# Optimization experiments

Hardware: AMD Instinct MI355X
Metric: run time of the kernel (lower is better)

## Reference

```python
import jax, jax.numpy as jnp
import numpy as np

H = 16
D_MODEL = 1024
D_K = D_MODEL // H
B, S = 2, 2048


def setup_inputs() -> dict:
    key = jax.random.key(0)
    ks = jax.random.split(key, 11)
    scale = 1.0 / np.sqrt(D_MODEL)
    inp = {
        "query": jax.random.normal(ks[0], (B, S, D_MODEL), jnp.float32),
        "key": jax.random.normal(ks[1], (B, S, D_MODEL), jnp.float32),
        "value": jax.random.normal(ks[2], (B, S, D_MODEL), jnp.float32),
        # four nn.Linear(d_model, d_model): Wq, Wk, Wv, Wo (torch convention: y = x @ W.T + b)
        "Wq": jax.random.uniform(ks[3], (D_MODEL, D_MODEL), jnp.float32, -scale, scale),
        "bq": jax.random.uniform(ks[4], (D_MODEL,), jnp.float32, -scale, scale),
        "Wk": jax.random.uniform(ks[5], (D_MODEL, D_MODEL), jnp.float32, -scale, scale),
        "bk": jax.random.uniform(ks[6], (D_MODEL,), jnp.float32, -scale, scale),
        "Wv": jax.random.uniform(ks[7], (D_MODEL, D_MODEL), jnp.float32, -scale, scale),
        "bv": jax.random.uniform(ks[8], (D_MODEL,), jnp.float32, -scale, scale),
        "Wo": jax.random.uniform(ks[9], (D_MODEL, D_MODEL), jnp.float32, -scale, scale),
        "bo": jax.random.uniform(ks[10], (D_MODEL,), jnp.float32, -scale, scale),
    }
    return inp


def _split_heads(x):
    # [B, S, D] -> [B, H, S, d_k]
    b, s, _ = x.shape
    return x.reshape(b, s, H, D_K).transpose(0, 2, 1, 3)


def reference(query, key, value, Wq, bq, Wk, bk, Wv, bv, Wo, bo):
    q = _split_heads(query @ Wq.T + bq)
    k = _split_heads(key @ Wk.T + bk)
    v = _split_heads(value @ Wv.T + bv)
    # scaled dot-product attention (dropout omitted: reference is eval-mode)
    scores = jnp.einsum("bhqd,bhkd->bhqk", q, k) / np.sqrt(D_K).astype(np.float32)
    p = jax.nn.softmax(scores, axis=-1)
    x = jnp.einsum("bhqk,bhkd->bhqd", p, v)
    x = x.transpose(0, 2, 1, 3).reshape(query.shape[0], -1, H * D_K)
    return x @ Wo.T + bo
```

## Files before the change

kernel.cpp:

```cpp
#include <hip/hip_runtime.h>

typedef unsigned short u16;
typedef unsigned int u32;
typedef __attribute__((ext_vector_type(8))) short short8;
typedef __attribute__((ext_vector_type(8))) _Float16 half8;
typedef __attribute__((ext_vector_type(4))) float floatx4;
typedef __attribute__((ext_vector_type(4))) unsigned short ushortx4;
typedef __attribute__((ext_vector_type(4))) unsigned int uint4v;

#define DEV static __device__ __forceinline__

DEV float bf2f(u16 u) { union { unsigned u; float f; } v; v.u = ((unsigned)u) << 16; return v.f; }
DEV u16 f2bf(float f) {
  union { float f; unsigned u; } v; v.f = f;
  return (u16)((v.u + 0x7FFFu + ((v.u >> 16) & 1u)) >> 16);
}
DEV u16 f2h(float f) { return __builtin_bit_cast(u16, (_Float16)f); }
DEV u32 pkh(float a, float b) {
  return __builtin_bit_cast(u32, __builtin_amdgcn_cvt_pkrtz(a, b));
}
DEV float fexp2(float x) { return __builtin_amdgcn_exp2f(x); }

#define GLDS(g, l) __builtin_amdgcn_global_load_lds( \
    (const __attribute__((address_space(1))) void*)(g), \
    (__attribute__((address_space(3))) void*)(l), 16, 0, 0)

struct CvtArg {
  const float* src[11];
  u16* dst[11];
  int cum[12];
};

__global__ void convert(CvtArg a) {
  const long base = ((long)blockIdx.x * 256 + threadIdx.x) * 4;
  if (base >= a.cum[11]) return;
  int s = 0;
  while (s < 10 && base >= a.cum[s + 1]) ++s;
  const long off = base - a.cum[s];
  const float* sp = a.src[s] + off;
  ushortx4 u;
#pragma unroll
  for (int r = 0; r < 4; ++r) u[r] = f2bf(sp[r]);
  *(ushortx4*)(a.dst[s] + off) = u;
}

struct GemmArg {
  const u16* x;
  const u16* w;
  const u16* bias;
  u16* dst;
  int mode;
};

__global__ __launch_bounds__(256, 2) void gemm_nt(GemmArg g0, GemmArg g1, GemmArg g2) {
  GemmArg g = (blockIdx.z == 0) ? g0 : ((blockIdx.z == 1) ? g1 : g2);
  __shared__ u16 As[2][128 * 32];
  __shared__ u16 Bs[2][128 * 32];
  const int tid = threadIdx.x, w = tid >> 6, l = tid & 63;
  const int l15 = l & 15, quad = l >> 4;
  const int bm = blockIdx.x, bn = blockIdx.y;
  const int wm = w >> 1, wn = w & 1;

  floatx4 acc[4][4];
#pragma unroll
  for (int i = 0; i < 4; ++i)
#pragma unroll
    for (int j = 0; j < 4; ++j) acc[i][j] = (floatx4){0.f, 0.f, 0.f, 0.f};

  const u16* xb = g.x + (long)(bm * 128 + w * 16 + (l >> 2)) * 1024 + (l & 3) * 8;
  const u16* wb = g.w + (long)(bn * 128 + w * 16 + (l >> 2)) * 1024 + (l & 3) * 8;
  const int sbo = (w * 16) * 32;

  for (int kt = 0; kt < 16; ++kt) {
    const int k0 = kt * 64;
    __syncthreads();
#pragma unroll
    for (int kc = 0; kc < 2; ++kc) {
#pragma unroll
      for (int p = 0; p < 2; ++p) {
        GLDS(xb + (long)p * 64 * 1024 + k0 + kc * 32, &As[kc][sbo + p * 64 * 32]);
        GLDS(wb + (long)p * 64 * 1024 + k0 + kc * 32, &Bs[kc][sbo + p * 64 * 32]);
      }
    }
    __syncthreads();
#pragma unroll
    for (int kc = 0; kc < 2; ++kc) {
      short8 af[4], bfr[4];
#pragma unroll
      for (int mi = 0; mi < 4; ++mi)
        af[mi] = *(const short8*)&As[kc][(wm * 64 + mi * 16 + l15) * 32 + quad * 8];
#pragma unroll
      for (int ni = 0; ni < 4; ++ni)
        bfr[ni] = *(const short8*)&Bs[kc][(wn * 64 + ni * 16 + l15) * 32 + quad * 8];
#pragma unroll
      for (int mi = 0; mi < 4; ++mi)
#pragma unroll
        for (int ni = 0; ni < 4; ++ni)
          acc[mi][ni] = __builtin_amdgcn_mfma_f32_16x16x32_bf16(af[mi], bfr[ni], acc[mi][ni], 0, 0, 0);
    }
  }

  float bv[4];
#pragma unroll
  for (int ni = 0; ni < 4; ++ni) bv[ni] = bf2f(g.bias[bn * 128 + wn * 64 + ni * 16 + l15]);

#pragma unroll
  for (int mi = 0; mi < 4; ++mi) {
    const int mbase = bm * 128 + wm * 64 + mi * 16 + quad * 4;
#pragma unroll
    for (int ni = 0; ni < 4; ++ni) {
      const int n = bn * 128 + wn * 64 + ni * 16 + l15;
      if (g.mode == 2) {
        const int b = mbase >> 11, s = mbase & 2047;
        const int h = n >> 6, d = n & 63;
        ushortx4 u;
#pragma unroll
        for (int r = 0; r < 4; ++r) u[r] = f2h(acc[mi][ni][r] + bv[ni]);
        *(ushortx4*)&g.dst[((long)(b * 16 + h) * 64 + d) * 2048 + s] = u;
      } else {
        const float sc = (g.mode == 0) ? 0.18033688011f : 1.0f;
        const int h = n >> 6, d = n & 63;
#pragma unroll
        for (int r = 0; r < 4; ++r) {
          const int m = mbase + r, b = m >> 11, s = m & 2047;
          g.dst[((long)(b * 16 + h) * 2048 + s) * 64 + d] = f2bf((acc[mi][ni][r] + bv[ni]) * sc);
        }
      }
    }
  }
}

__global__ __launch_bounds__(256, 2) void gemm_o(const u16* __restrict__ x,
                                                 const u16* __restrict__ wo,
                                                 const u16* __restrict__ bias,
                                                 float* __restrict__ dst) {
  const int bid = blockIdx.x;
  const int gidx = (bid & 7) * 64 + (bid >> 3);
  const int bm = gidx & 63;
  const int bn = gidx >> 6;

  __shared__ u16 As[2][64 * 32];
  __shared__ u16 Bs[2][128 * 32];
  const int tid = threadIdx.x, w = tid >> 6, l = tid & 63;
  const int l15 = l & 15, quad = l >> 4;
  const int wm = w >> 1, wn = w & 1;

  floatx4 acc[2][4];
#pragma unroll
  for (int i = 0; i < 2; ++i)
#pragma unroll
    for (int j = 0; j < 4; ++j) acc[i][j] = (floatx4){0.f, 0.f, 0.f, 0.f};

  const u16* xb = x + (long)(bm * 64 + w * 16 + (l >> 2)) * 1024 + (l & 3) * 8;
  const u16* wb = wo + (long)(bn * 128 + w * 16 + (l >> 2)) * 1024 + (l & 3) * 8;
  const int sbo = (w * 16) * 32;

  for (int kt = 0; kt < 16; ++kt) {
    const int k0 = kt * 64;
    __syncthreads();
#pragma unroll
    for (int kc = 0; kc < 2; ++kc) {
      GLDS(xb + k0 + kc * 32, &As[kc][sbo]);
#pragma unroll
      for (int p = 0; p < 2; ++p)
        GLDS(wb + (long)p * 64 * 1024 + k0 + kc * 32, &Bs[kc][sbo + p * 64 * 32]);
    }
    __syncthreads();
#pragma unroll
    for (int kc = 0; kc < 2; ++kc) {
      short8 af[2], bfr[4];
#pragma unroll
      for (int mi = 0; mi < 2; ++mi)
        af[mi] = *(const short8*)&As[kc][(wm * 32 + mi * 16 + l15) * 32 + quad * 8];
#pragma unroll
      for (int ni = 0; ni < 4; ++ni)
        bfr[ni] = *(const short8*)&Bs[kc][(wn * 64 + ni * 16 + l15) * 32 + quad * 8];
#pragma unroll
      for (int mi = 0; mi < 2; ++mi)
#pragma unroll
        for (int ni = 0; ni < 4; ++ni)
          acc[mi][ni] = __builtin_amdgcn_mfma_f32_16x16x32_bf16(af[mi], bfr[ni], acc[mi][ni], 0, 0, 0);
    }
  }

  float bv[4];
#pragma unroll
  for (int ni = 0; ni < 4; ++ni) bv[ni] = bf2f(bias[bn * 128 + wn * 64 + ni * 16 + l15]);

#pragma unroll
  for (int mi = 0; mi < 2; ++mi) {
    const int mbase = bm * 64 + wm * 32 + mi * 16 + quad * 4;
#pragma unroll
    for (int ni = 0; ni < 4; ++ni) {
      const int n = bn * 128 + wn * 64 + ni * 16 + l15;
#pragma unroll
      for (int r = 0; r < 4; ++r)
        dst[(long)(mbase + r) * 1024 + n] = acc[mi][ni][r] + bv[ni];
    }
  }
}

__global__ __launch_bounds__(256, 2) void attn_flash(const u16* __restrict__ Q,
                                                     const u16* __restrict__ K,
                                                     const u16* __restrict__ V,
                                                     u16* __restrict__ X) {
  __shared__ u16 KVs[4][64 * 72];
  const int tid = threadIdx.x, w = tid >> 6, l = tid & 63;
  const int l15 = l & 15, quad = l >> 4;
  const int qh = w >> 1, kh = w & 1;

  const int bid = blockIdx.x;
  const int xcd = bid & 7, idx = bid >> 3;
  const int qx = idx & 15, bh = xcd + 8 * (idx >> 4);
  const int q0 = qx * 128;

  const u16* qp = Q + (long)bh * 2048 * 64;
  const u16* kp = K + (long)bh * 2048 * 64;
  const u16* vp = V + (long)bh * 2048 * 64;

  const int r0 = tid >> 3, c0 = tid & 7, r1 = 32 + (tid >> 3);

  short8 skA0, svA0, skA1, svA1, skB0, svB0, skB1, svB1;

#define ISSUE_LOADS_A(kv0) \
    skA0 = *(const short8*)(kp + (long)((kv0) + r0) * 64 + c0 * 8); \
    svA0 = *(const short8*)(vp + (long)r0 * 2048 + (kv0) + c0 * 8); \
    skA1 = *(const short8*)(kp + (long)((kv0) + r1) * 64 + c0 * 8); \
    svA1 = *(const short8*)(vp + (long)r1 * 2048 + (kv0) + c0 * 8);

#define ISSUE_LOADS_B(kv0) \
    skB0 = *(const short8*)(kp + (long)((kv0) + r0) * 64 + c0 * 8); \
    svB0 = *(const short8*)(vp + (long)r0 * 2048 + (kv0) + c0 * 8); \
    skB1 = *(const short8*)(kp + (long)((kv0) + r1) * 64 + c0 * 8); \
    svB1 = *(const short8*)(vp + (long)r1 * 2048 + (kv0) + c0 * 8);

#define STORE_TILE_A(pb_) \
    *(short8*)&KVs[pb_][r0 * 72 + c0 * 8] = skA0; \
    *(short8*)&KVs[2 + (pb_)][r0 * 72 + c0 * 8] = svA0; \
    *(short8*)&KVs[pb_][r1 * 72 + c0 * 8] = skA1; \
    *(short8*)&KVs[2 + (pb_)][r1 * 72 + c0 * 8] = svA1;

#define STORE_TILE_B(pb_) \
    *(short8*)&KVs[pb_][r0 * 72 + c0 * 8] = skB0; \
    *(short8*)&KVs[2 + (pb_)][r0 * 72 + c0 * 8] = svB0; \
    *(short8*)&KVs[pb_][r1 * 72 + c0 * 8] = skB1; \
    *(short8*)&KVs[2 + (pb_)][r1 * 72 + c0 * 8] = svB1;

  short8 qf[4][2];
#pragma unroll
  for (int nq = 0; nq < 4; ++nq)
#pragma unroll
    for (int kc = 0; kc < 2; ++kc)
      qf[nq][kc] = *(const short8*)(qp + (long)(q0 + qh * 64 + nq * 16 + l15) * 64 + kc * 32 + quad * 8);

  floatx4 o[4][4];
#pragma unroll
  for (int nq = 0; nq < 4; ++nq)
#pragma unroll
    for (int nd = 0; nd < 4; ++nd) o[nq][nd] = (floatx4){0.f, 0.f, 0.f, 0.f};
  float den[4] = {0.f, 0.f, 0.f, 0.f};

  const bool p1 = (l & 32) != 0;
  const bool p3 = (l & 16) != 0;
  const bool p2 = p1 ^ p3;

#define BFLY(pbv, m00, m01, m10, m11) { \
    u32 A0 = p1 ? (m10) : (m00), A1 = p1 ? (m11) : (m01); \
    u32 s0_ = p1 ? (m00) : (m10), s1_ = p1 ? (m01) : (m11); \
    u32 B0 = (u32)__shfl_xor((int)s0_, 32), B1 = (u32)__shfl_xor((int)s1_, 32); \
    u32 t0 = p2 ? A0 : B0, t1 = p2 ? A1 : B1; \
    u32 u0 = (u32)__shfl_xor((int)t0, 16), u1 = (u32)__shfl_xor((int)t1, 16); \
    u32 w0 = p2 ? B0 : A0, w1 = p2 ? B1 : A1; \
    pbv[0] = p3 ? u0 : w0; pbv[1] = p3 ? u1 : w1; \
    pbv[2] = p3 ? w0 : u0; pbv[3] = p3 ? w1 : u1; \
  }

#define ATTN_ITER(t, p, IS, ST) { \
    if ((t) < 30) { IS(((t) + 2) * 64) } \
    if ((t) < 31) { ST((p) ^ 1) } \
    const int kr0 = kh * 32 + l15, kr1 = kh * 32 + 16 + l15; \
    short8 ak00 = *(const short8*)&KVs[p][kr0 * 72 + quad * 8]; \
    short8 ak01 = *(const short8*)&KVs[p][kr0 * 72 + 32 + quad * 8]; \
    short8 ak10 = *(const short8*)&KVs[p][kr1 * 72 + quad * 8]; \
    short8 ak11 = *(const short8*)&KVs[p][kr1 * 72 + 32 + quad * 8]; \
    half8 vf0 = *(const half8*)&KVs[2 + (p)][(0 * 16 + l15) * 72 + kh * 32 + quad * 8]; \
    half8 vf1 = *(const half8*)&KVs[2 + (p)][(1 * 16 + l15) * 72 + kh * 32 + quad * 8]; \
    half8 vf2 = *(const half8*)&KVs[2 + (p)][(2 * 16 + l15) * 72 + kh * 32 + quad * 8]; \
    half8 vf3 = *(const half8*)&KVs[2 + (p)][(3 * 16 + l15) * 72 + kh * 32 + quad * 8]; \
    u32 pk[4][2][2]; \
    _Pragma("unroll") \
    for (int nq = 0; nq < 4; ++nq) { \
      floatx4 st0 = (floatx4){0.f, 0.f, 0.f, 0.f}, st1 = (floatx4){0.f, 0.f, 0.f, 0.f}; \
      st0 = __builtin_amdgcn_mfma_f32_16x16x32_bf16(ak00, qf[nq][0], st0, 0, 0, 0); \
      st0 = __builtin_amdgcn_mfma_f32_16x16x32_bf16(ak01, qf[nq][1], st0, 0, 0, 0); \
      st1 = __builtin_amdgcn_mfma_f32_16x16x32_bf16(ak10, qf[nq][0], st1, 0, 0, 0); \
      st1 = __builtin_amdgcn_mfma_f32_16x16x32_bf16(ak11, qf[nq][1], st1, 0, 0, 0); \
      float e0 = fexp2(st0[0]), e1 = fexp2(st0[1]), e2 = fexp2(st0[2]), e3 = fexp2(st0[3]); \
      den[nq] += (e0 + e1) + (e2 + e3); \
      pk[nq][0][0] = pkh(e0, e1); pk[nq][0][1] = pkh(e2, e3); \
      e0 = fexp2(st1[0]); e1 = fexp2(st1[1]); e2 = fexp2(st1[2]); e3 = fexp2(st1[3]); \
      den[nq] += (e0 + e1) + (e2 + e3); \
      pk[nq][1][0] = pkh(e0, e1); pk[nq][1][1] = pkh(e2, e3); \
    } \
    _Pragma("unroll") \
    for (int nq = 0; nq < 4; ++nq) { \
      uint4v pb; \
      BFLY(pb, pk[nq][0][0], pk[nq][0][1], pk[nq][1][0], pk[nq][1][1]) \
      half8 pbs = __builtin_bit_cast(half8, pb); \
      o[nq][0] = __builtin_amdgcn_mfma_f32_16x16x32_f16(vf0, pbs, o[nq][0], 0, 0, 0); \
      o[nq][1] = __builtin_amdgcn_mfma_f32_16x16x32_f16(vf1, pbs, o[nq][1], 0, 0, 0); \
      o[nq][2] = __builtin_amdgcn_mfma_f32_16x16x32_f16(vf2, pbs, o[nq][2], 0, 0, 0); \
      o[nq][3] = __builtin_amdgcn_mfma_f32_16x16x32_f16(vf3, pbs, o[nq][3], 0, 0, 0); \
    } \
    __syncthreads(); \
  }

  ISSUE_LOADS_A(0)
  STORE_TILE_A(0)
  ISSUE_LOADS_B(64)
  __syncthreads();

  for (int tt = 0; tt < 32; tt += 2) {
    ATTN_ITER(tt, 0, ISSUE_LOADS_A, STORE_TILE_B)
    ATTN_ITER(tt + 1, 1, ISSUE_LOADS_B, STORE_TILE_A)
  }

  float dsum[4];
#pragma unroll
  for (int nq = 0; nq < 4; ++nq) {
    float d = den[nq];
    d += __shfl_xor(d, 16);
    d += __shfl_xor(d, 32);
    dsum[nq] = d;
  }

  float* osc = (float*)KVs;
  float* dsc = osc + 8192;
  if (kh == 1) {
#pragma unroll
    for (int nq = 0; nq < 4; ++nq)
#pragma unroll
      for (int nd = 0; nd < 4; ++nd)
        *(floatx4*)&osc[(((qh * 4 + nq) * 4 + nd) * 64 + l) * 4] = o[nq][nd];
    if (l < 16) {
#pragma unroll
      for (int nq = 0; nq < 4; ++nq) dsc[(qh * 4 + nq) * 16 + l] = dsum[nq];
    }
  }
  __syncthreads();

  if (kh == 0) {
    float rcp[4];
#pragma unroll
    for (int nq = 0; nq < 4; ++nq) rcp[nq] = 1.0f / (dsum[nq] + dsc[(qh * 4 + nq) * 16 + l15]);
    const int b = bh >> 4, h = bh & 15;
#pragma unroll
    for (int nq = 0; nq < 4; ++nq) {
      const int s = q0 + qh * 64 + nq * 16 + l15;
      u16* xrow = X + ((long)(b * 2048 + s)) * 1024 + h * 64;
#pragma unroll
      for (int nd = 0; nd < 4; ++nd) {
        floatx4 om = o[nq][nd] + *(const floatx4*)&osc[(((qh * 4 + nq) * 4 + nd) * 64 + l) * 4];
        ushortx4 u;
#pragma unroll
        for (int r = 0; r < 4; ++r) u[r] = f2bf(om[r] * rcp[nq]);
        *(ushortx4*)&xrow[nd * 16 + quad * 4] = u;
      }
    }
  }
}

extern "C" void kernel_launch(void* const* d_in, const int* in_sizes, int n_in,
                              void* d_out, int out_size, void* d_ws, size_t ws_size,
                              hipStream_t stream) {
  u16* ws = (u16*)d_ws;
  const size_t M1 = 1048576, M4 = 4194304;
  u16* NQ  = ws;
  u16* NK  = ws + M4;
  u16* NV  = ws + 2 * M4;
  u16* NWQ = ws + 3 * M4;
  u16* NWK = ws + 3 * M4 + M1;
  u16* NWV = ws + 3 * M4 + 2 * M1;
  u16* NWO = ws + 3 * M4 + 3 * M1;
  u16* NBQ = ws + 3 * M4 + 4 * M1;
  u16* NBK = NBQ + 1024;
  u16* NBV = NBQ + 2048;
  u16* NBO = NBQ + 3072;
  u16* Qb = ws + 16 * M1 + 8192;
  u16* Kb = Qb + M4;
  u16* Vb = Qb + 2 * M4;
  u16* Xb = NQ;

  CvtArg ca;
  u16* dsts[11] = {NQ, NK, NV, NWQ, NBQ, NWK, NBK, NWV, NBV, NWO, NBO};
  int sizes[11] = {(int)M4, (int)M4, (int)M4, (int)M1, 1024, (int)M1, 1024, (int)M1, 1024, (int)M1, 1024};
  int c = 0;
  for (int i = 0; i < 11; ++i) {
    ca.src[i] = (const float*)d_in[i];
    ca.dst[i] = dsts[i];
    ca.cum[i] = c;
    c += sizes[i];
  }
  ca.cum[11] = c;
  convert<<<(c / 4 + 255) / 256, 256, 0, stream>>>(ca);

  GemmArg gq{NQ, NWQ, NBQ, Qb, 0};
  GemmArg gk{NK, NWK, NBK, Kb, 1};
  GemmArg gv{NV, NWV, NBV, Vb, 2};
  gemm_nt<<<dim3(32, 8, 3), 256, 0, stream>>>(gq, gk, gv);

  attn_flash<<<dim3(512), 256, 0, stream>>>(Qb, Kb, Vb, Xb);

  gemm_o<<<dim3(512), 256, 0, stream>>>(Xb, NWO, NBO, (float*)d_out);
}
```

Measured before the change: 218.8 us.

## Load K/V fragments directly from global into registers, removing LDS staging

Replaces the shared-memory double-buffered K/V tiles with per-wave register double buffers loaded straight from global memory in MFMA fragment layout. This removes LDS writes and reads and the per-iteration block barrier. In exchange, waves redundantly fetch overlapping K/V data, and V loads become strided 16-byte accesses that rely on cache hits. The LDS buffer is reduced to the output-reduction scratch.

```diff
diff --git a/kernel.cpp b/kernel.cpp
--- a/kernel.cpp
+++ b/kernel.cpp
@@ -204,7 +204,7 @@
                                                      const u16* __restrict__ K,
                                                      const u16* __restrict__ V,
                                                      u16* __restrict__ X) {
-  __shared__ u16 KVs[4][64 * 72];
+  __shared__ float osc[8 * 4 * 64 * 4 + 128];
   const int tid = threadIdx.x, w = tid >> 6, l = tid & 63;
   const int l15 = l & 15, quad = l >> 4;
   const int qh = w >> 1, kh = w & 1;
@@ -218,40 +218,15 @@
   const u16* kp = K + (long)bh * 2048 * 64;
   const u16* vp = V + (long)bh * 2048 * 64;
 
-  const int r0 = tid >> 3, c0 = tid & 7, r1 = 32 + (tid >> 3);
-
-  short8 skA0, svA0, skA1, svA1, skB0, svB0, skB1, svB1;
-
-#define ISSUE_LOADS_A(kv0) \
-    skA0 = *(const short8*)(kp + (long)((kv0) + r0) * 64 + c0 * 8); \
-    svA0 = *(const short8*)(vp + (long)r0 * 2048 + (kv0) + c0 * 8); \
-    skA1 = *(const short8*)(kp + (long)((kv0) + r1) * 64 + c0 * 8); \
-    svA1 = *(const short8*)(vp + (long)r1 * 2048 + (kv0) + c0 * 8);
-
-#define ISSUE_LOADS_B(kv0) \
-    skB0 = *(const short8*)(kp + (long)((kv0) + r0) * 64 + c0 * 8); \
-    svB0 = *(const short8*)(vp + (long)r0 * 2048 + (kv0) + c0 * 8); \
-    skB1 = *(const short8*)(kp + (long)((kv0) + r1) * 64 + c0 * 8); \
-    svB1 = *(const short8*)(vp + (long)r1 * 2048 + (kv0) + c0 * 8);
-
-#define STORE_TILE_A(pb_) \
-    *(short8*)&KVs[pb_][r0 * 72 + c0 * 8] = skA0; \
-    *(short8*)&KVs[2 + (pb_)][r0 * 72 + c0 * 8] = svA0; \
-    *(short8*)&KVs[pb_][r1 * 72 + c0 * 8] = skA1; \
-    *(short8*)&KVs[2 + (pb_)][r1 * 72 + c0 * 8] = svA1;
-
-#define STORE_TILE_B(pb_) \
-    *(short8*)&KVs[pb_][r0 * 72 + c0 * 8] = skB0; \
-    *(short8*)&KVs[2 + (pb_)][r0 * 72 + c0 * 8] = svB0; \
-    *(short8*)&KVs[pb_][r1 * 72 + c0 * 8] = skB1; \
-    *(short8*)&KVs[2 + (pb_)][r1 * 72 + c0 * 8] = svB1;
-
   short8 qf[4][2];
 #pragma unroll
   for (int nq = 0; nq < 4; ++nq)
 #pragma unroll
     for (int kc = 0; kc < 2; ++kc)
       qf[nq][kc] = *(const short8*)(qp + (long)(q0 + qh * 64 + nq * 16 + l15) * 64 + kc * 32 + quad * 8);
+
+  const u16* kbase = kp + (long)(kh * 32 + l15) * 64 + quad * 8;
+  const u16* vbase = vp + (long)l15 * 2048 + kh * 32 + quad * 8;
 
   floatx4 o[4][4];
 #pragma unroll
@@ -275,26 +250,32 @@
     pbv[2] = p3 ? w0 : u0; pbv[3] = p3 ? w1 : u1; \
   }
 
-#define ATTN_ITER(t, p, IS, ST) { \
-    if ((t) < 30) { IS(((t) + 2) * 64) } \
-    if ((t) < 31) { ST((p) ^ 1) } \
-    const int kr0 = kh * 32 + l15, kr1 = kh * 32 + 16 + l15; \
-    short8 ak00 = *(const short8*)&KVs[p][kr0 * 72 + quad * 8]; \
-    short8 ak01 = *(const short8*)&KVs[p][kr0 * 72 + 32 + quad * 8]; \
-    short8 ak10 = *(const short8*)&KVs[p][kr1 * 72 + quad * 8]; \
-    short8 ak11 = *(const short8*)&KVs[p][kr1 * 72 + 32 + quad * 8]; \
-    half8 vf0 = *(const half8*)&KVs[2 + (p)][(0 * 16 + l15) * 72 + kh * 32 + quad * 8]; \
-    half8 vf1 = *(const half8*)&KVs[2 + (p)][(1 * 16 + l15) * 72 + kh * 32 + quad * 8]; \
-    half8 vf2 = *(const half8*)&KVs[2 + (p)][(2 * 16 + l15) * 72 + kh * 32 + quad * 8]; \
-    half8 vf3 = *(const half8*)&KVs[2 + (p)][(3 * 16 + l15) * 72 + kh * 32 + quad * 8]; \
+  short8 kA[4], kB[4];
+  half8 vA[4], vB[4];
+
+#define LOADF(KS, VS, t_) { \
+    const u16* kt_ = kbase + (long)(t_) * 64 * 64; \
+    KS[0] = *(const short8*)(kt_); \
+    KS[1] = *(const short8*)(kt_ + 32); \
+    KS[2] = *(const short8*)(kt_ + 16 * 64); \
+    KS[3] = *(const short8*)(kt_ + 16 * 64 + 32); \
+    const u16* vt_ = vbase + (t_) * 64; \
+    VS[0] = *(const half8*)(vt_); \
+    VS[1] = *(const half8*)(vt_ + 16 * 2048); \
+    VS[2] = *(const half8*)(vt_ + 32 * 2048); \
+    VS[3] = *(const half8*)(vt_ + 48 * 2048); \
+  }
+
+#define ATTN_ITER(KS, VS, KN, VN, t_) { \
+    if ((t_) + 1 < 32) LOADF(KN, VN, (t_) + 1) \
     u32 pk[4][2][2]; \
     _Pragma("unroll") \
     for (int nq = 0; nq < 4; ++nq) { \
       floatx4 st0 = (floatx4){0.f, 0.f, 0.f, 0.f}, st1 = (floatx4){0.f, 0.f, 0.f, 0.f}; \
-      st0 = __builtin_amdgcn_mfma_f32_16x16x32_bf16(ak00, qf[nq][0], st0, 0, 0, 0); \
-      st0 = __builtin_amdgcn_mfma_f32_16x16x32_bf16(ak01, qf[nq][1], st0, 0, 0, 0); \
-      st1 = __builtin_amdgcn_mfma_f32_16x16x32_bf16(ak10, qf[nq][0], st1, 0, 0, 0); \
-      st1 = __builtin_amdgcn_mfma_f32_16x16x32_bf16(ak11, qf[nq][1], st1, 0, 0, 0); \
+      st0 = __builtin_amdgcn_mfma_f32_16x16x32_bf16(KS[0], qf[nq][0], st0, 0, 0, 0); \
+      st0 = __builtin_amdgcn_mfma_f32_16x16x32_bf16(KS[1], qf[nq][1], st0, 0, 0, 0); \
+      st1 = __builtin_amdgcn_mfma_f32_16x16x32_bf16(KS[2], qf[nq][0], st1, 0, 0, 0); \
+      st1 = __builtin_amdgcn_mfma_f32_16x16x32_bf16(KS[3], qf[nq][1], st1, 0, 0, 0); \
       float e0 = fexp2(st0[0]), e1 = fexp2(st0[1]), e2 = fexp2(st0[2]), e3 = fexp2(st0[3]); \
       den[nq] += (e0 + e1) + (e2 + e3); \
       pk[nq][0][0] = pkh(e0, e1); pk[nq][0][1] = pkh(e2, e3); \
@@ -307,22 +288,17 @@
       uint4v pb; \
       BFLY(pb, pk[nq][0][0], pk[nq][0][1], pk[nq][1][0], pk[nq][1][1]) \
       half8 pbs = __builtin_bit_cast(half8, pb); \
-      o[nq][0] = __builtin_amdgcn_mfma_f32_16x16x32_f16(vf0, pbs, o[nq][0], 0, 0, 0); \
-      o[nq][1] = __builtin_amdgcn_mfma_f32_16x16x32_f16(vf1, pbs, o[nq][1], 0, 0, 0); \
-      o[nq][2] = __builtin_amdgcn_mfma_f32_16x16x32_f16(vf2, pbs, o[nq][2], 0, 0, 0); \
-      o[nq][3] = __builtin_amdgcn_mfma_f32_16x16x32_f16(vf3, pbs, o[nq][3], 0, 0, 0); \
+      o[nq][0] = __builtin_amdgcn_mfma_f32_16x16x32_f16(VS[0], pbs, o[nq][0], 0, 0, 0); \
+      o[nq][1] = __builtin_amdgcn_mfma_f32_16x16x32_f16(VS[1], pbs, o[nq][1], 0, 0, 0); \
+      o[nq][2] = __builtin_amdgcn_mfma_f32_16x16x32_f16(VS[2], pbs, o[nq][2], 0, 0, 0); \
+      o[nq][3] = __builtin_amdgcn_mfma_f32_16x16x32_f16(VS[3], pbs, o[nq][3], 0, 0, 0); \
     } \
-    __syncthreads(); \
-  }
-
-  ISSUE_LOADS_A(0)
-  STORE_TILE_A(0)
-  ISSUE_LOADS_B(64)
-  __syncthreads();
-
+  }
+
+  LOADF(kA, vA, 0)
   for (int tt = 0; tt < 32; tt += 2) {
-    ATTN_ITER(tt, 0, ISSUE_LOADS_A, STORE_TILE_B)
-    ATTN_ITER(tt + 1, 1, ISSUE_LOADS_B, STORE_TILE_A)
+    ATTN_ITER(kA, vA, kB, vB, tt)
+    ATTN_ITER(kB, vB, kA, vA, tt + 1)
   }
 
   float dsum[4];
@@ -334,7 +310,6 @@
     dsum[nq] = d;
   }
 
-  float* osc = (float*)KVs;
   float* dsc = osc + 8192;
   if (kh == 1) {
 #pragma unroll
```

New measurement: 235.3 us. +7.6%, slower.

## Process two KV tiles per barrier with a four-slot LDS ring

Applied to the files above, without the earlier changes.

Enlarges the K/V shared-memory ring from two slots to four, and restructures the attention loop so each iteration stores two prefetched tiles, issues global loads for the two tiles after that, then computes two tiles before a single barrier. This halves the number of __syncthreads per KV sweep and raises the global-load prefetch distance. In exchange LDS usage doubles, which may limit occupancy alongside the output scratch reuse.

```diff
diff --git a/kernel.cpp b/kernel.cpp
--- a/kernel.cpp
+++ b/kernel.cpp
@@ -204,7 +204,7 @@
                                                      const u16* __restrict__ K,
                                                      const u16* __restrict__ V,
                                                      u16* __restrict__ X) {
-  __shared__ u16 KVs[4][64 * 72];
+  __shared__ u16 KVs[8][64 * 72];
   const int tid = threadIdx.x, w = tid >> 6, l = tid & 63;
   const int l15 = l & 15, quad = l >> 4;
   const int qh = w >> 1, kh = w & 1;
@@ -234,17 +234,17 @@
     skB1 = *(const short8*)(kp + (long)((kv0) + r1) * 64 + c0 * 8); \
     svB1 = *(const short8*)(vp + (long)r1 * 2048 + (kv0) + c0 * 8);
 
-#define STORE_TILE_A(pb_) \
-    *(short8*)&KVs[pb_][r0 * 72 + c0 * 8] = skA0; \
-    *(short8*)&KVs[2 + (pb_)][r0 * 72 + c0 * 8] = svA0; \
-    *(short8*)&KVs[pb_][r1 * 72 + c0 * 8] = skA1; \
-    *(short8*)&KVs[2 + (pb_)][r1 * 72 + c0 * 8] = svA1;
-
-#define STORE_TILE_B(pb_) \
-    *(short8*)&KVs[pb_][r0 * 72 + c0 * 8] = skB0; \
-    *(short8*)&KVs[2 + (pb_)][r0 * 72 + c0 * 8] = svB0; \
-    *(short8*)&KVs[pb_][r1 * 72 + c0 * 8] = skB1; \
-    *(short8*)&KVs[2 + (pb_)][r1 * 72 + c0 * 8] = svB1;
+#define STORE_TILE_A(kb_) \
+    *(short8*)&KVs[kb_][r0 * 72 + c0 * 8] = skA0; \
+    *(short8*)&KVs[4 + (kb_)][r0 * 72 + c0 * 8] = svA0; \
+    *(short8*)&KVs[kb_][r1 * 72 + c0 * 8] = skA1; \
+    *(short8*)&KVs[4 + (kb_)][r1 * 72 + c0 * 8] = svA1;
+
+#define STORE_TILE_B(kb_) \
+    *(short8*)&KVs[kb_][r0 * 72 + c0 * 8] = skB0; \
+    *(short8*)&KVs[4 + (kb_)][r0 * 72 + c0 * 8] = svB0; \
+    *(short8*)&KVs[kb_][r1 * 72 + c0 * 8] = skB1; \
+    *(short8*)&KVs[4 + (kb_)][r1 * 72 + c0 * 8] = svB1;
 
   short8 qf[4][2];
 #pragma unroll
@@ -275,18 +275,16 @@
     pbv[2] = p3 ? w0 : u0; pbv[3] = p3 ? w1 : u1; \
   }
 
-#define ATTN_ITER(t, p, IS, ST) { \
-    if ((t) < 30) { IS(((t) + 2) * 64) } \
-    if ((t) < 31) { ST((p) ^ 1) } \
+#define COMPUTE(kb_) { \
     const int kr0 = kh * 32 + l15, kr1 = kh * 32 + 16 + l15; \
-    short8 ak00 = *(const short8*)&KVs[p][kr0 * 72 + quad * 8]; \
-    short8 ak01 = *(const short8*)&KVs[p][kr0 * 72 + 32 + quad * 8]; \
-    short8 ak10 = *(const short8*)&KVs[p][kr1 * 72 + quad * 8]; \
-    short8 ak11 = *(const short8*)&KVs[p][kr1 * 72 + 32 + quad * 8]; \
-    half8 vf0 = *(const half8*)&KVs[2 + (p)][(0 * 16 + l15) * 72 + kh * 32 + quad * 8]; \
-    half8 vf1 = *(const half8*)&KVs[2 + (p)][(1 * 16 + l15) * 72 + kh * 32 + quad * 8]; \
-    half8 vf2 = *(const half8*)&KVs[2 + (p)][(2 * 16 + l15) * 72 + kh * 32 + quad * 8]; \
-    half8 vf3 = *(const half8*)&KVs[2 + (p)][(3 * 16 + l15) * 72 + kh * 32 + quad * 8]; \
+    short8 ak00 = *(const short8*)&KVs[kb_][kr0 * 72 + quad * 8]; \
+    short8 ak01 = *(const short8*)&KVs[kb_][kr0 * 72 + 32 + quad * 8]; \
+    short8 ak10 = *(const short8*)&KVs[kb_][kr1 * 72 + quad * 8]; \
+    short8 ak11 = *(const short8*)&KVs[kb_][kr1 * 72 + 32 + quad * 8]; \
+    half8 vf0 = *(const half8*)&KVs[4 + (kb_)][(0 * 16 + l15) * 72 + kh * 32 + quad * 8]; \
+    half8 vf1 = *(const half8*)&KVs[4 + (kb_)][(1 * 16 + l15) * 72 + kh * 32 + quad * 8]; \
+    half8 vf2 = *(const half8*)&KVs[4 + (kb_)][(2 * 16 + l15) * 72 + kh * 32 + quad * 8]; \
+    half8 vf3 = *(const half8*)&KVs[4 + (kb_)][(3 * 16 + l15) * 72 + kh * 32 + quad * 8]; \
     u32 pk[4][2][2]; \
     _Pragma("unroll") \
     for (int nq = 0; nq < 4; ++nq) { \
@@ -312,17 +310,24 @@
       o[nq][2] = __builtin_amdgcn_mfma_f32_16x16x32_f16(vf2, pbs, o[nq][2], 0, 0, 0); \
       o[nq][3] = __builtin_amdgcn_mfma_f32_16x16x32_f16(vf3, pbs, o[nq][3], 0, 0, 0); \
     } \
-    __syncthreads(); \
   }
 
   ISSUE_LOADS_A(0)
   STORE_TILE_A(0)
   ISSUE_LOADS_B(64)
+  STORE_TILE_B(1)
+  ISSUE_LOADS_A(2 * 64)
+  ISSUE_LOADS_B(3 * 64)
   __syncthreads();
 
   for (int tt = 0; tt < 32; tt += 2) {
-    ATTN_ITER(tt, 0, ISSUE_LOADS_A, STORE_TILE_B)
-    ATTN_ITER(tt + 1, 1, ISSUE_LOADS_B, STORE_TILE_A)
+    if (tt + 2 < 32) { STORE_TILE_A((tt + 2) & 3) }
+    if (tt + 3 < 32) { STORE_TILE_B((tt + 3) & 3) }
+    if (tt + 4 < 32) { ISSUE_LOADS_A((tt + 4) * 64) }
+    if (tt + 5 < 32) { ISSUE_LOADS_B((tt + 5) * 64) }
+    COMPUTE(tt & 3)
+    COMPUTE((tt + 1) & 3)
+    __syncthreads();
   }
 
   float dsum[4];
```

New measurement: 221.2 us. Within noise of the previous version (+1.1%).
